# Optimization experiments

Hardware: AMD Instinct MI355X
Metric: run time of the kernel (lower is better)

Reference implementation:

```python
import jax, jax.numpy as jnp
import numpy as np

T = 32          # n_node_types
EXTRA = 3       # input_dim = T + 3
D = 9           # perfect binary tree depth -> N = 2**D - 1 = 511 nodes/plan
N = 2 ** D - 1
EMB = 64
HID = 64
FC = 64
OUT = 8         # N_METRICS
NS = 5          # N_SAMPLES
P = 2560        # number of plans (P // NS = 512 groups)
B = 512


def setup_inputs() -> dict:
    key = jax.random.key(0)
    ks = jax.random.split(key, 8)

    def lin(k, o, i):
        return (jax.random.normal(k, (o, i), jnp.float32) / np.sqrt(i)).astype(jnp.float32)

    x0 = jax.random.normal(ks[0], (P, N, T + EXTRA), jnp.float32)
    x = jax.random.uniform(ks[1], (B, P // NS), jnp.float32)
    return {
        "x": x,
        "x0": x0,
        "W_emb": lin(ks[2], EMB, T), "b_emb": jnp.zeros((EMB,), jnp.float32),
        "W0": lin(ks[3], HID, EMB + EXTRA), "b0": jnp.zeros((HID,), jnp.float32),
        "W1": lin(ks[4], HID, EMB + EXTRA + 2 * HID), "b1": jnp.zeros((HID,), jnp.float32),
        "Wfc1": lin(ks[5], FC, HID), "bfc1": jnp.zeros((FC,), jnp.float32),
        "Wfc2": lin(ks[6], OUT, FC), "bfc2": jnp.zeros((OUT,), jnp.float32),
    }


def reference(x, x0, W_emb, b_emb, W0, b0, W1, b1, Wfc1, bfc1, Wfc2, bfc2):
    # --- enc_dnn: per-node embed + concat(extra, children hiddens) + Linear + ReLU ---
    # node_emb = emb(xi[:T]); node_input = [node_emb, xi[T:], h_children...]
    emb = jnp.einsum('pnt,et->pne', x0[..., :T], W_emb) + b_emb    # [P,N,EMB]
    feats = jnp.concatenate([emb, x0[..., T:]], axis=-1)           # [P,N,EMB+3]
    # heap layout: node i's children are 2i+1, 2i+2; level l occupies [2^l-1, 2^{l+1}-1)
    lo = 2 ** (D - 1) - 1
    h = jax.nn.relu(jnp.einsum('pnf,hf->pnh', feats[:, lo:], W0) + b0)  # leaves
    for l in range(D - 2, -1, -1):  # structural loop over tree levels (fixed, small)
        lo, n = 2 ** l - 1, 2 ** l
        f = feats[:, lo:lo + n]
        inp = jnp.concatenate([f, h[:, 0::2], h[:, 1::2]], axis=-1)  # [emb|extra|h_left|h_right]
        h = jax.nn.relu(jnp.einsum('pnf,hf->pnh', inp, W1) + b1)
    h0 = h[:, 0]                                                   # root hidden, [P,HID]
    # --- agg_weight ---
    mean_h = h0.reshape(-1, NS, HID).mean(axis=1)                  # [P/NS, HID]
    weighted = x @ mean_h                                          # [B, HID]
    hid = jax.nn.relu(weighted @ Wfc1.T + bfc1)
    return hid @ Wfc2.T + bfc2                                     # [B, OUT]
```

## Files before the change

kernel.cpp:

```cpp
#include <hip/hip_runtime.h>
#include <hip/hip_bf16.h>


typedef __attribute__((ext_vector_type(8))) short s8v;
typedef __attribute__((ext_vector_type(4))) float f4v;
typedef unsigned short u16;

__device__ __forceinline__ u16 f2bf(float f) {
    return __builtin_bit_cast(u16, __float2bfloat16(f));
}
__device__ __forceinline__ f4v mfma16(s8v a, s8v b, f4v c) {
    return __builtin_amdgcn_mfma_f32_16x16x32_bf16(a, b, c, 0, 0, 0);
}
#define SWZ(r) ((((r) & 1) | (((r) >> 1) & 6)) << 3)

__device__ __forceinline__ s8v xtail_lds(const u16* xr, int lq) {
    s8v v = *(const s8v*)(xr + 32);
    if (lq != 0) v = (s8v){0,0,0,0,0,0,0,0};
    return v;
}

__global__ void prep_kernel(const float* __restrict__ W_emb, const float* __restrict__ b_emb,
                            const float* __restrict__ W0, const float* __restrict__ b0,
                            const float* __restrict__ W1, const float* __restrict__ b1,
                            u16* __restrict__ wt1, u16* __restrict__ wt0,
                            float* __restrict__ b1p, float* __restrict__ b0p)
{
    int idx = blockIdx.x * 256 + threadIdx.x;
    if (idx < 64 * 192) {
        int h = idx / 192, k = idx % 192;
        float v;
        if (k < 32) { v = 0.f; for (int e = 0; e < 64; e++) v = fmaf(W1[h*195+e], W_emb[e*32+k], v); }
        else if (k < 35)  v = W1[h*195 + 64 + (k - 32)];
        else if (k < 64)  v = 0.f;
        else              v = W1[h*195 + 67 + (k - 64)];
        wt1[h*192 + k] = f2bf(v);
    } else if (idx < 64*192 + 64*64) {
        int j = idx - 64*192; int h = j >> 6, k = j & 63;
        float v;
        if (k < 32)      { v = 0.f; for (int e = 0; e < 64; e++) v = fmaf(W0[h*67+e], W_emb[e*32+k], v); }
        else if (k < 35)   v = W0[h*67 + 64 + (k - 32)];
        else               v = 0.f;
        wt0[h*64 + k] = f2bf(v);
    } else if (idx < 64*192 + 64*64 + 64) {
        int h = idx - (64*192 + 64*64);
        float v = b1[h];
        for (int e = 0; e < 64; e++) v = fmaf(W1[h*195+e], b_emb[e], v);
        b1p[h] = v;
    } else if (idx < 64*192 + 64*64 + 128) {
        int h = idx - (64*192 + 64*64 + 64);
        float v = b0[h];
        for (int e = 0; e < 64; e++) v = fmaf(W0[h*67+e], b_emb[e], v);
        b0p[h] = v;
    }
}

__global__ __launch_bounds__(512, 4) void tree_front(
    const float* __restrict__ x0,
    const u16* __restrict__ wt1, const u16* __restrict__ wt0,
    const float* __restrict__ b1p, const float* __restrict__ b0p,
    u16* __restrict__ h4)
{
    __shared__ __align__(16) u16 xleaf[257 * 40];
    __shared__ __align__(16) u16 xmid [129 * 40];
    __shared__ __align__(16) u16 buf0[256 * 64];
    __shared__ __align__(16) u16 buf1[128 * 64];

    const int tid = threadIdx.x;
    const int l  = tid & 63;
    const int w  = tid >> 6;
    const int c2 = w & 1;
    const int wr = w >> 1;
    const int lq = l >> 4;
    const int lm = l & 15;
    const int p  = blockIdx.x;
    const float* xg = x0 + (size_t)p * 511 * 35;

    auto BAR = []() {
        asm volatile("s_waitcnt lgkmcnt(0)" ::: "memory");
        __builtin_amdgcn_s_barrier();
        asm volatile("" ::: "memory");
    };

    float sA[18], sB[9], sC[9];
    const float* gA = xg + 255 * 35;
    #pragma unroll
    for (int t = 0; t < 18; t++) { int i = t*512 + tid; sA[t] = (i < 8960) ? gA[i] : 0.f; }
    const float* gB = xg + 127 * 35;
    #pragma unroll
    for (int t = 0; t < 9; t++)  { int i = t*512 + tid; sB[t] = (i < 4480) ? gB[i] : 0.f; }
    const float* gC = xg;
    #pragma unroll
    for (int t = 0; t < 9; t++)  { int i = t*512 + tid; sC[t] = (i < 4445) ? gC[i] : 0.f; }

    if (tid < 256) {
        int b = tid * 40;
        for (int c = 35; c < 40; c++) xleaf[b + c] = 0;
        if (tid == 255) {
            for (int c = 0; c < 40; c++) xleaf[256 * 40 + c] = 0;
        }
    } else if (tid < 384) {
        int b = (tid - 256) * 40;
        for (int c = 35; c < 40; c++) xmid[b + c] = 0;
        if (tid == 383) {
            for (int c = 0; c < 40; c++) xmid[128 * 40 + c] = 0;
        }
    }

    s8v wL[2][2]; f4v bi0[2];
    #pragma unroll
    for (int cc = 0; cc < 2; cc++) {
        int col = c2*32 + cc*16 + lm;
        wL[cc][0] = *(const s8v*)(wt0 + col*64 +      lq*8);
        wL[cc][1] = *(const s8v*)(wt0 + col*64 + 32 + lq*8);
        float bv = b0p[col];
        bi0[cc] = (f4v){bv, bv, bv, bv};
    }

    #pragma unroll
    for (int t = 0; t < 18; t++) {
        int i = t*512 + tid;
        if (i < 8960) { int row = i / 35, col = i - row*35; xleaf[row*40 + col] = f2bf(sA[t]); }
    }
    BAR();

    auto store16 = [&](u16* bufW, int R0, const f4v& acc0, const f4v& acc1) {
        #pragma unroll
        for (int r = 0; r < 4; r++) {
            int ro = R0 + lq * 4 + r;
            int sw = SWZ(ro);
            bufW[ro*64 + ((c2*32      + lm) ^ sw)] = f2bf(fmaxf(acc0[r], 0.f));
            bufW[ro*64 + ((c2*32 + 16 + lm) ^ sw)] = f2bf(fmaxf(acc1[r], 0.f));
        }
    };

    #pragma unroll
    for (int t = 0; t < 4; t++) {
        int R0 = (wr + 4*t) * 16;
        const u16* xr = xleaf + (R0 + lm) * 40;
        s8v a0 = *(const s8v*)(xr + lq*8);
        s8v a1 = xtail_lds(xr, lq);
        f4v acc0 = bi0[0], acc1 = bi0[1];
        acc0 = mfma16(a0, wL[0][0], acc0);
        acc1 = mfma16(a0, wL[1][0], acc1);
        acc0 = mfma16(a1, wL[0][1], acc0);
        acc1 = mfma16(a1, wL[1][1], acc1);
        store16(buf0, R0, acc0, acc1);
    }

    s8v wX[2][2], wH[2][4]; f4v bi1[2];
    #pragma unroll
    for (int cc = 0; cc < 2; cc++) {
        int col = c2*32 + cc*16 + lm;
        #pragma unroll
        for (int ks = 0; ks < 2; ks++) wX[cc][ks] = *(const s8v*)(wt1 + col*192 + ks*32 + lq*8);
        #pragma unroll
        for (int ks = 0; ks < 4; ks++) wH[cc][ks] = *(const s8v*)(wt1 + col*192 + 64 + ks*32 + lq*8);
        float bv = b1p[col];
        bi1[cc] = (f4v){bv, bv, bv, bv};
    }

    #pragma unroll
    for (int t = 0; t < 9; t++) {
        int i = t*512 + tid;
        if (i < 4480) { int row = i / 35, col = i - row*35; xmid[row*40 + col] = f2bf(sB[t]); }
    }
    BAR();

    auto ctile = [&](const u16* bufR, u16* bufW, const u16* xb, int xr0, int R0) {
        const u16* xr = xb + (xr0 + lm) * 40;
        s8v a0 = *(const s8v*)(xr + lq*8);
        s8v a1 = xtail_lds(xr, lq);
        f4v acc0 = bi1[0], acc1 = bi1[1];
        acc0 = mfma16(a0, wX[0][0], acc0);
        acc1 = mfma16(a0, wX[1][0], acc1);
        acc0 = mfma16(a1, wX[0][1], acc0);
        acc1 = mfma16(a1, wX[1][1], acc1);
        int g = R0 + lm;
        #pragma unroll
        for (int ks = 0; ks < 4; ks++) {
            int k0 = ks*32 + lq*8;
            int rr = 2*g + (k0 >> 6);
            s8v a = *(const s8v*)(bufR + rr*64 + ((k0 & 63) ^ SWZ(rr)));
            acc0 = mfma16(a, wH[0][ks], acc0);
            acc1 = mfma16(a, wH[1][ks], acc1);
        }
        store16(bufW, R0, acc0, acc1);
    };

    ctile(buf0, buf1, xmid, wr * 16,        wr * 16);
    ctile(buf0, buf1, xmid, (wr + 4) * 16,  (wr + 4) * 16);

    #pragma unroll
    for (int t = 0; t < 9; t++) {
        int i = t*512 + tid;
        if (i < 4445) { int row = i / 35, col = i - row*35; xleaf[row*40 + col] = f2bf(sC[t]); }
    }
    BAR();

    ctile(buf1, buf0, xleaf, 63 + wr * 16, wr * 16);
    BAR();
    if (wr < 2) ctile(buf0, buf1, xleaf, 31 + wr * 16, wr * 16);
    BAR();
    if (wr == 0) {
        const u16* xr = xleaf + (15 + lm) * 40;
        s8v a0 = *(const s8v*)(xr + lq*8);
        s8v a1 = xtail_lds(xr, lq);
        f4v acc0 = bi1[0], acc1 = bi1[1];
        acc0 = mfma16(a0, wX[0][0], acc0);
        acc1 = mfma16(a0, wX[1][0], acc1);
        acc0 = mfma16(a1, wX[0][1], acc0);
        acc1 = mfma16(a1, wX[1][1], acc1);
        #pragma unroll
        for (int ks = 0; ks < 4; ks++) {
            int k0 = ks*32 + lq*8;
            int rr = 2*lm + (k0 >> 6);
            s8v a = *(const s8v*)(buf1 + rr*64 + ((k0 & 63) ^ SWZ(rr)));
            acc0 = mfma16(a, wH[0][ks], acc0);
            acc1 = mfma16(a, wH[1][ks], acc1);
        }
        #pragma unroll
        for (int r = 0; r < 4; r++) {
            h4[((size_t)p*16 + lq*4 + r) * 64 + c2*32      + lm] = f2bf(fmaxf(acc0[r], 0.f));
            h4[((size_t)p*16 + lq*4 + r) * 64 + c2*32 + 16 + lm] = f2bf(fmaxf(acc1[r], 0.f));
        }
    }
}

struct XL { float4 A, B, T; };
__device__ __forceinline__ s8v mk0(const XL& v) {
    s8v r;
    r[0]=(short)f2bf(v.A.x); r[1]=(short)f2bf(v.A.y); r[2]=(short)f2bf(v.A.z); r[3]=(short)f2bf(v.A.w);
    r[4]=(short)f2bf(v.B.x); r[5]=(short)f2bf(v.B.y); r[6]=(short)f2bf(v.B.z); r[7]=(short)f2bf(v.B.w);
    return r;
}
__device__ __forceinline__ s8v mk1(const XL& v) {
    s8v r = {0,0,0,0,0,0,0,0};
    r[0]=(short)f2bf(v.T.y); r[1]=(short)f2bf(v.T.z); r[2]=(short)f2bf(v.T.w);
    return r;
}

__global__ __launch_bounds__(64) void k3_tail(
    const float* __restrict__ x0,
    const u16* __restrict__ wt1, const float* __restrict__ b1p,
    const u16* __restrict__ h4, float* __restrict__ h0)
{
    __shared__ __align__(16) u16 tb0[32 * 64];
    __shared__ __align__(16) u16 tb1[32 * 64];
    const int l  = threadIdx.x;
    const int lq = l >> 4, lm = l & 15;
    const int p  = blockIdx.x;
    const float* xb = x0 + (size_t)p * 511 * 35;

    auto xload = [&](int lo) -> XL {
        const float* xr = xb + (size_t)(lo + lm) * 35;
        XL v;
        v.A = *(const float4*)(xr + lq * 8);
        v.B = *(const float4*)(xr + lq * 8 + 4);
        if (lq == 0) v.T = *(const float4*)(xr + 31);
        else         v.T = float4{0.f, 0.f, 0.f, 0.f};
        return v;
    };

    XL X3 = xload(7), X2 = xload(3), X1 = xload(1), X0v = xload(0);
    s8v ch[4];
    #pragma unroll
    for (int ks = 0; ks < 4; ks++) {
        int k0 = ks*32 + lq*8;
        int rr = 2*lm + (k0 >> 6);
        ch[ks] = *(const s8v*)(h4 + ((size_t)p*16 + rr)*64 + (k0 & 63));
    }

    s8v wB[6][4]; f4v bi[4];
    #pragma unroll
    for (int ct = 0; ct < 4; ct++) {
        int col = ct*16 + lm;
        #pragma unroll
        for (int ks = 0; ks < 6; ks++) wB[ks][ct] = *(const s8v*)(wt1 + col*192 + ks*32 + lq*8);
        float bv = b1p[col];
        bi[ct] = (f4v){bv, bv, bv, bv};
    }

    f4v acc[4];
    auto store_lds = [&](u16* buf) {
        #pragma unroll
        for (int r = 0; r < 4; r++) {
            int ro = lq*4 + r; int sw = SWZ(ro);
            #pragma unroll
            for (int ct = 0; ct < 4; ct++)
                buf[ro*64 + ((ct*16 + lm) ^ sw)] = f2bf(fmaxf(acc[ct][r], 0.f));
        }
        asm volatile("s_waitcnt lgkmcnt(0)" ::: "memory");
    };

    {
        s8v a0 = mk0(X3), a1 = mk1(X3);
        #pragma unroll
        for (int ct = 0; ct < 4; ct++) {
            acc[ct] = bi[ct];
            acc[ct] = mfma16(a0, wB[0][ct], acc[ct]);
            acc[ct] = mfma16(a1, wB[1][ct], acc[ct]);
        }
        #pragma unroll
        for (int ks = 0; ks < 4; ks++)
            #pragma unroll
            for (int ct = 0; ct < 4; ct++) acc[ct] = mfma16(ch[ks], wB[2 + ks][ct], acc[ct]);
        store_lds(tb0);
    }

    auto level = [&](const XL& xv, const u16* bufR) {
        s8v a0 = mk0(xv), a1 = mk1(xv);
        #pragma unroll
        for (int ct = 0; ct < 4; ct++) {
            acc[ct] = bi[ct];
            acc[ct] = mfma16(a0, wB[0][ct], acc[ct]);
            acc[ct] = mfma16(a1, wB[1][ct], acc[ct]);
        }
        #pragma unroll
        for (int ks = 0; ks < 4; ks++) {
            int k0 = ks*32 + lq*8;
            int rr = 2*lm + (k0 >> 6);
            s8v a = *(const s8v*)(bufR + rr*64 + ((k0 & 63) ^ SWZ(rr)));
            #pragma unroll
            for (int ct = 0; ct < 4; ct++) acc[ct] = mfma16(a, wB[2 + ks][ct], acc[ct]);
        }
    };
    level(X2, tb0); store_lds(tb1);
    level(X1, tb1); store_lds(tb0);
    level(X0v, tb0);
    if (lq == 0) {
        #pragma unroll
        for (int ct = 0; ct < 4; ct++)
            h0[(size_t)p*64 + ct*16 + lm] = fmaxf(acc[ct][0], 0.f);
    }
}

__global__ void mean_kernel(const float* __restrict__ h0, float* __restrict__ mh)
{
    int idx = blockIdx.x * blockDim.x + threadIdx.x;
    if (idx < 512 * 64) {
        int g = idx >> 6, h = idx & 63;
        float s = 0.f;
        #pragma unroll
        for (int q = 0; q < 5; q++) s += h0[(size_t)(g * 5 + q) * 64 + h];
        mh[idx] = s * 0.2f;
    }
}

__global__ __launch_bounds__(64) void head_kernel(const float* __restrict__ x,
                                                  const float* __restrict__ mh,
                                                  const float* __restrict__ Wfc1,
                                                  const float* __restrict__ bfc1,
                                                  const float* __restrict__ Wfc2,
                                                  const float* __restrict__ bfc2,
                                                  float* __restrict__ out)
{
    __shared__ float sw[64];
    __shared__ float sh[64];
    int b = blockIdx.x, h = threadIdx.x;

    float a0 = 0.f, a1 = 0.f, a2 = 0.f, a3 = 0.f;
    const float* xr = x + (size_t)b * 512;
    for (int g = 0; g < 512; g += 4) {
        a0 = fmaf(xr[g + 0], mh[(g + 0) * 64 + h], a0);
        a1 = fmaf(xr[g + 1], mh[(g + 1) * 64 + h], a1);
        a2 = fmaf(xr[g + 2], mh[(g + 2) * 64 + h], a2);
        a3 = fmaf(xr[g + 3], mh[(g + 3) * 64 + h], a3);
    }
    sw[h] = (a0 + a1) + (a2 + a3);
    __syncthreads();

    float acc = bfc1[h];
    #pragma unroll 8
    for (int k = 0; k < 64; k++) acc = fmaf(Wfc1[h * 64 + k], sw[k], acc);
    sh[h] = fmaxf(acc, 0.f);
    __syncthreads();

    if (h < 8) {
        float o = bfc2[h];
        #pragma unroll 8
        for (int f = 0; f < 64; f++) o = fmaf(Wfc2[h * 64 + f], sh[f], o);
        out[(size_t)b * 8 + h] = o;
    }
}

extern "C" void kernel_launch(void* const* d_in, const int* in_sizes, int n_in,
                              void* d_out, int out_size, void* d_ws, size_t ws_size,
                              hipStream_t stream)
{
    (void)in_sizes; (void)n_in; (void)out_size; (void)ws_size;
    const float* x     = (const float*)d_in[0];
    const float* x0    = (const float*)d_in[1];
    const float* W_emb = (const float*)d_in[2];
    const float* b_emb = (const float*)d_in[3];
    const float* W0    = (const float*)d_in[4];
    const float* b0    = (const float*)d_in[5];
    const float* W1    = (const float*)d_in[6];
    const float* b1    = (const float*)d_in[7];
    const float* Wfc1  = (const float*)d_in[8];
    const float* bfc1  = (const float*)d_in[9];
    const float* Wfc2  = (const float*)d_in[10];
    const float* bfc2  = (const float*)d_in[11];
    float* out = (float*)d_out;

    u16* wt1   = (u16*)d_ws;
    u16* wt0   = wt1 + 64 * 192;
    float* b1p = (float*)(wt0 + 64 * 64);
    float* b0p = b1p + 64;
    u16* h4    = (u16*)(b0p + 64);
    float* h0  = (float*)(h4 + (size_t)2560 * 16 * 64);
    float* mh  = h0 + 2560 * 64;

    prep_kernel<<<65, 256, 0, stream>>>(W_emb, b_emb, W0, b0, W1, b1, wt1, wt0, b1p, b0p);
    tree_front<<<2560, 512, 0, stream>>>(x0, wt1, wt0, b1p, b0p, h4);
    k3_tail<<<2560, 64, 0, stream>>>(x0, wt1, b1p, h4, h0);
    mean_kernel<<<128, 256, 0, stream>>>(h0, mh);
    head_kernel<<<512, 64, 0, stream>>>(x, mh, Wfc1, bfc1, Wfc2, bfc2, out);
}
```

Measured before the change: 104.2 us.

## Make tree_front persistent over five plans with software-prefetched x0 loads

```diff
diff --git a/kernel.cpp b/kernel.cpp
--- a/kernel.cpp
+++ b/kernel.cpp
@@ -73,8 +73,6 @@
     const int wr = w >> 1;
     const int lq = l >> 4;
     const int lm = l & 15;
-    const int p  = blockIdx.x;
-    const float* xg = x0 + (size_t)p * 511 * 35;
 
     auto BAR = []() {
         asm volatile("s_waitcnt lgkmcnt(0)" ::: "memory");
@@ -82,47 +80,66 @@
         asm volatile("" ::: "memory");
     };
 
-    float sA[18], sB[9], sC[9];
-    const float* gA = xg + 255 * 35;
-    #pragma unroll
-    for (int t = 0; t < 18; t++) { int i = t*512 + tid; sA[t] = (i < 8960) ? gA[i] : 0.f; }
-    const float* gB = xg + 127 * 35;
-    #pragma unroll
-    for (int t = 0; t < 9; t++)  { int i = t*512 + tid; sB[t] = (i < 4480) ? gB[i] : 0.f; }
-    const float* gC = xg;
-    #pragma unroll
-    for (int t = 0; t < 9; t++)  { int i = t*512 + tid; sC[t] = (i < 4445) ? gC[i] : 0.f; }
-
     if (tid < 256) {
         int b = tid * 40;
         for (int c = 35; c < 40; c++) xleaf[b + c] = 0;
-        if (tid == 255) {
-            for (int c = 0; c < 40; c++) xleaf[256 * 40 + c] = 0;
-        }
+        if (tid == 255) { for (int c = 0; c < 40; c++) xleaf[256 * 40 + c] = 0; }
     } else if (tid < 384) {
         int b = (tid - 256) * 40;
         for (int c = 35; c < 40; c++) xmid[b + c] = 0;
-        if (tid == 383) {
-            for (int c = 0; c < 40; c++) xmid[128 * 40 + c] = 0;
-        }
-    }
-
-    s8v wL[2][2]; f4v bi0[2];
+        if (tid == 383) { for (int c = 0; c < 40; c++) xmid[128 * 40 + c] = 0; }
+    }
+
+    s8v wX[2][2], wH[2][4]; f4v bi1[2];
     #pragma unroll
     for (int cc = 0; cc < 2; cc++) {
         int col = c2*32 + cc*16 + lm;
-        wL[cc][0] = *(const s8v*)(wt0 + col*64 +      lq*8);
-        wL[cc][1] = *(const s8v*)(wt0 + col*64 + 32 + lq*8);
-        float bv = b0p[col];
-        bi0[cc] = (f4v){bv, bv, bv, bv};
-    }
-
-    #pragma unroll
-    for (int t = 0; t < 18; t++) {
-        int i = t*512 + tid;
-        if (i < 8960) { int row = i / 35, col = i - row*35; xleaf[row*40 + col] = f2bf(sA[t]); }
-    }
-    BAR();
+        #pragma unroll
+        for (int ks = 0; ks < 2; ks++) wX[cc][ks] = *(const s8v*)(wt1 + col*192 + ks*32 + lq*8);
+        #pragma unroll
+        for (int ks = 0; ks < 4; ks++) wH[cc][ks] = *(const s8v*)(wt1 + col*192 + 64 + ks*32 + lq*8);
+        float bv = b1p[col];
+        bi1[cc] = (f4v){bv, bv, bv, bv};
+    }
+
+    float sA[18], sB[9], sC[9];
+    const float* xg = x0 + (size_t)(blockIdx.x * 5) * 511 * 35;
+
+    auto issueA = [&](const float* g) {
+        const float* gA = g + 255 * 35;
+        #pragma unroll
+        for (int t = 0; t < 18; t++) { int i = t*512 + tid; sA[t] = (i < 8960) ? gA[i] : 0.f; }
+    };
+    auto issueB = [&](const float* g) {
+        const float* gB = g + 127 * 35;
+        #pragma unroll
+        for (int t = 0; t < 9; t++)  { int i = t*512 + tid; sB[t] = (i < 4480) ? gB[i] : 0.f; }
+    };
+    auto issueC = [&](const float* g) {
+        #pragma unroll
+        for (int t = 0; t < 9; t++)  { int i = t*512 + tid; sC[t] = (i < 4445) ? g[i] : 0.f; }
+    };
+    auto writeA = [&]() {
+        #pragma unroll
+        for (int t = 0; t < 18; t++) {
+            int i = t*512 + tid;
+            if (i < 8960) { int row = i / 35, col = i - row*35; xleaf[row*40 + col] = f2bf(sA[t]); }
+        }
+    };
+    auto writeB = [&]() {
+        #pragma unroll
+        for (int t = 0; t < 9; t++) {
+            int i = t*512 + tid;
+            if (i < 4480) { int row = i / 35, col = i - row*35; xmid[row*40 + col] = f2bf(sB[t]); }
+        }
+    };
+    auto writeC = [&]() {
+        #pragma unroll
+        for (int t = 0; t < 9; t++) {
+            int i = t*512 + tid;
+            if (i < 4445) { int row = i / 35, col = i - row*35; xleaf[row*40 + col] = f2bf(sC[t]); }
+        }
+    };
 
     auto store16 = [&](u16* bufW, int R0, const f4v& acc0, const f4v& acc1) {
         #pragma unroll
@@ -133,40 +150,6 @@
             bufW[ro*64 + ((c2*32 + 16 + lm) ^ sw)] = f2bf(fmaxf(acc1[r], 0.f));
         }
     };
-
-    #pragma unroll
-    for (int t = 0; t < 4; t++) {
-        int R0 = (wr + 4*t) * 16;
-        const u16* xr = xleaf + (R0 + lm) * 40;
-        s8v a0 = *(const s8v*)(xr + lq*8);
-        s8v a1 = xtail_lds(xr, lq);
-        f4v acc0 = bi0[0], acc1 = bi0[1];
-        acc0 = mfma16(a0, wL[0][0], acc0);
-        acc1 = mfma16(a0, wL[1][0], acc1);
-        acc0 = mfma16(a1, wL[0][1], acc0);
-        acc1 = mfma16(a1, wL[1][1], acc1);
-        store16(buf0, R0, acc0, acc1);
-    }
-
-    s8v wX[2][2], wH[2][4]; f4v bi1[2];
-    #pragma unroll
-    for (int cc = 0; cc < 2; cc++) {
-        int col = c2*32 + cc*16 + lm;
-        #pragma unroll
-        for (int ks = 0; ks < 2; ks++) wX[cc][ks] = *(const s8v*)(wt1 + col*192 + ks*32 + lq*8);
-        #pragma unroll
-        for (int ks = 0; ks < 4; ks++) wH[cc][ks] = *(const s8v*)(wt1 + col*192 + 64 + ks*32 + lq*8);
-        float bv = b1p[col];
-        bi1[cc] = (f4v){bv, bv, bv, bv};
-    }
-
-    #pragma unroll
-    for (int t = 0; t < 9; t++) {
-        int i = t*512 + tid;
-        if (i < 4480) { int row = i / 35, col = i - row*35; xmid[row*40 + col] = f2bf(sB[t]); }
-    }
-    BAR();
-
     auto ctile = [&](const u16* bufR, u16* bufW, const u16* xb, int xr0, int R0) {
         const u16* xr = xb + (xr0 + lm) * 40;
         s8v a0 = *(const s8v*)(xr + lq*8);
@@ -188,42 +171,83 @@
         store16(bufW, R0, acc0, acc1);
     };
 
-    ctile(buf0, buf1, xmid, wr * 16,        wr * 16);
-    ctile(buf0, buf1, xmid, (wr + 4) * 16,  (wr + 4) * 16);
-
-    #pragma unroll
-    for (int t = 0; t < 9; t++) {
-        int i = t*512 + tid;
-        if (i < 4445) { int row = i / 35, col = i - row*35; xleaf[row*40 + col] = f2bf(sC[t]); }
-    }
-    BAR();
-
-    ctile(buf1, buf0, xleaf, 63 + wr * 16, wr * 16);
-    BAR();
-    if (wr < 2) ctile(buf0, buf1, xleaf, 31 + wr * 16, wr * 16);
-    BAR();
-    if (wr == 0) {
-        const u16* xr = xleaf + (15 + lm) * 40;
-        s8v a0 = *(const s8v*)(xr + lq*8);
-        s8v a1 = xtail_lds(xr, lq);
-        f4v acc0 = bi1[0], acc1 = bi1[1];
-        acc0 = mfma16(a0, wX[0][0], acc0);
-        acc1 = mfma16(a0, wX[1][0], acc1);
-        acc0 = mfma16(a1, wX[0][1], acc0);
-        acc1 = mfma16(a1, wX[1][1], acc1);
-        #pragma unroll
-        for (int ks = 0; ks < 4; ks++) {
-            int k0 = ks*32 + lq*8;
-            int rr = 2*lm + (k0 >> 6);
-            s8v a = *(const s8v*)(buf1 + rr*64 + ((k0 & 63) ^ SWZ(rr)));
-            acc0 = mfma16(a, wH[0][ks], acc0);
-            acc1 = mfma16(a, wH[1][ks], acc1);
-        }
-        #pragma unroll
-        for (int r = 0; r < 4; r++) {
-            h4[((size_t)p*16 + lq*4 + r) * 64 + c2*32      + lm] = f2bf(fmaxf(acc0[r], 0.f));
-            h4[((size_t)p*16 + lq*4 + r) * 64 + c2*32 + 16 + lm] = f2bf(fmaxf(acc1[r], 0.f));
-        }
+    issueA(xg); issueB(xg); issueC(xg);
+
+    #pragma unroll 1
+    for (int it = 0; it < 5; it++) {
+        const int p = blockIdx.x * 5 + it;
+        const float* xgn = xg + 511 * 35;
+
+        s8v wL[2][2]; f4v bi0[2];
+        #pragma unroll
+        for (int cc = 0; cc < 2; cc++) {
+            int col = c2*32 + cc*16 + lm;
+            wL[cc][0] = *(const s8v*)(wt0 + col*64 +      lq*8);
+            wL[cc][1] = *(const s8v*)(wt0 + col*64 + 32 + lq*8);
+            float bv = b0p[col];
+            bi0[cc] = (f4v){bv, bv, bv, bv};
+        }
+
+        writeA();
+        BAR();
+
+        #pragma unroll
+        for (int t = 0; t < 4; t++) {
+            int R0 = (wr + 4*t) * 16;
+            const u16* xr = xleaf + (R0 + lm) * 40;
+            s8v a0 = *(const s8v*)(xr + lq*8);
+            s8v a1 = xtail_lds(xr, lq);
+            f4v acc0 = bi0[0], acc1 = bi0[1];
+            acc0 = mfma16(a0, wL[0][0], acc0);
+            acc1 = mfma16(a0, wL[1][0], acc1);
+            acc0 = mfma16(a1, wL[0][1], acc0);
+            acc1 = mfma16(a1, wL[1][1], acc1);
+            store16(buf0, R0, acc0, acc1);
+        }
+
+        if (it < 4) issueA(xgn);
+
+        writeB();
+        BAR();
+
+        ctile(buf0, buf1, xmid, wr * 16,       wr * 16);
+        ctile(buf0, buf1, xmid, (wr + 4) * 16, (wr + 4) * 16);
+
+        writeC();
+        BAR();
+
+        ctile(buf1, buf0, xleaf, 63 + wr * 16, wr * 16);
+
+        if (it < 4) { issueB(xgn); issueC(xgn); }
+
+        BAR();
+        if (wr < 2) ctile(buf0, buf1, xleaf, 31 + wr * 16, wr * 16);
+        BAR();
+        if (wr == 0) {
+            const u16* xr = xleaf + (15 + lm) * 40;
+            s8v a0 = *(const s8v*)(xr + lq*8);
+            s8v a1 = xtail_lds(xr, lq);
+            f4v acc0 = bi1[0], acc1 = bi1[1];
+            acc0 = mfma16(a0, wX[0][0], acc0);
+            acc1 = mfma16(a0, wX[1][0], acc1);
+            acc0 = mfma16(a1, wX[0][1], acc0);
+            acc1 = mfma16(a1, wX[1][1], acc1);
+            #pragma unroll
+            for (int ks = 0; ks < 4; ks++) {
+                int k0 = ks*32 + lq*8;
+                int rr = 2*lm + (k0 >> 6);
+                s8v a = *(const s8v*)(buf1 + rr*64 + ((k0 & 63) ^ SWZ(rr)));
+                acc0 = mfma16(a, wH[0][ks], acc0);
+                acc1 = mfma16(a, wH[1][ks], acc1);
+            }
+            #pragma unroll
+            for (int r = 0; r < 4; r++) {
+                h4[((size_t)p*16 + lq*4 + r) * 64 + c2*32      + lm] = f2bf(fmaxf(acc0[r], 0.f));
+                h4[((size_t)p*16 + lq*4 + r) * 64 + c2*32 + 16 + lm] = f2bf(fmaxf(acc1[r], 0.f));
+            }
+        }
+        BAR();
+        xg = xgn;
     }
 }
 
@@ -412,7 +436,7 @@
     float* mh  = h0 + 2560 * 64;
 
     prep_kernel<<<65, 256, 0, stream>>>(W_emb, b_emb, W0, b0, W1, b1, wt1, wt0, b1p, b0p);
-    tree_front<<<2560, 512, 0, stream>>>(x0, wt1, wt0, b1p, b0p, h4);
+    tree_front<<<512, 512, 0, stream>>>(x0, wt1, wt0, b1p, b0p, h4);
     k3_tail<<<2560, 64, 0, stream>>>(x0, wt1, b1p, h4, h0);
     mean_kernel<<<128, 256, 0, stream>>>(h0, mh);
     head_kernel<<<512, 64, 0, stream>>>(x, mh, Wfc1, bfc1, Wfc2, bfc2, out);
```

After: 279.6 us. 168% more time.
